# Kernel optimization log

Hardware: AMD Instinct MI355X
Metric: run time of the kernel (lower is better)

The kernel has to match this reference:

```python
import jax, jax.numpy as jnp
import numpy as np

H = 64  # hidden size
IN = 21  # input features

def setup_inputs() -> dict:
    key = jax.random.key(0)
    ks = jax.random.split(key, 12)
    s = 0.1
    B, T = 512, 3000
    return {
        "x":      jax.random.normal(ks[0], (B, T, IN), dtype=jnp.float32),
        # layer 0 (input 21 -> hidden 64); PyTorch gate order: i, f, g, o
        "Wih0":   jax.random.normal(ks[1], (4 * H, IN), dtype=jnp.float32) * s,
        "Whh0":   jax.random.normal(ks[2], (4 * H, H), dtype=jnp.float32) * s,
        "bih0":   jax.random.normal(ks[3], (4 * H,), dtype=jnp.float32) * s,
        "bhh0":   jax.random.normal(ks[4], (4 * H,), dtype=jnp.float32) * s,
        # layer 1 (hidden 64 -> hidden 64)
        "Wih1":   jax.random.normal(ks[5], (4 * H, H), dtype=jnp.float32) * s,
        "Whh1":   jax.random.normal(ks[6], (4 * H, H), dtype=jnp.float32) * s,
        "bih1":   jax.random.normal(ks[7], (4 * H,), dtype=jnp.float32) * s,
        "bhh1":   jax.random.normal(ks[8], (4 * H,), dtype=jnp.float32) * s,
        # final linear 64 -> 1
        "Wfc":    jax.random.normal(ks[9], (1, H), dtype=jnp.float32) * s,
        "bfc":    jax.random.normal(ks[10], (1,), dtype=jnp.float32) * s,
    }

def _lstm_layer(x_seq, Wih, Whh, bih, bhh):
    # x_seq: [B, T, F]. Precompute input projections for all timesteps (one big GEMM).
    xg = jnp.einsum('btf,gf->btg', x_seq, Wih) + (bih + bhh)  # [B, T, 4H]
    xg = jnp.transpose(xg, (1, 0, 2))  # [T, B, 4H] for scan over time
    B = x_seq.shape[0]
    h0 = jnp.zeros((B, H), dtype=x_seq.dtype)
    c0 = jnp.zeros((B, H), dtype=x_seq.dtype)

    def step(carry, xg_t):
        h, c = carry
        gates = xg_t + h @ Whh.T  # [B, 4H]
        i = jax.nn.sigmoid(gates[:, 0 * H:1 * H])
        f = jax.nn.sigmoid(gates[:, 1 * H:2 * H])
        g = jnp.tanh(gates[:, 2 * H:3 * H])
        o = jax.nn.sigmoid(gates[:, 3 * H:4 * H])
        c = f * c + i * g
        h = o * jnp.tanh(c)
        return (h, c), h

    (_, _), h_seq = jax.lax.scan(step, (h0, c0), xg)  # h_seq: [T, B, H]
    return jnp.transpose(h_seq, (1, 0, 2))  # [B, T, H]

def reference(x, Wih0, Whh0, bih0, bhh0, Wih1, Whh1, bih1, bhh1, Wfc, bfc):
    # 2-layer LSTM (eval mode: inter-layer dropout inactive), last timestep -> linear.
    h1 = _lstm_layer(x, Wih0, Whh0, bih0, bhh0)   # [B, T, H]
    h2 = _lstm_layer(h1, Wih1, Whh1, bih1, bhh1)  # [B, T, H]
    last = h2[:, -1, :]                            # [B, H]
    return last @ Wfc.T + bfc                      # [B, 1]
```

## Files before the change

### kernel.cpp

```cpp
#include <hip/hip_runtime.h>
#include <stdint.h>

namespace {

constexpr int NIN = 21;
constexpr int T   = 3000;
constexpr int NB  = 2;

typedef _Float16 f16x8 __attribute__((ext_vector_type(8)));
typedef float    f32x4 __attribute__((ext_vector_type(4)));

__device__ __forceinline__ float frcp(float x){ return __builtin_amdgcn_rcpf(x); }
__device__ __forceinline__ float sigm(float v){ return frcp(1.0f + __expf(-v)); }
__device__ __forceinline__ float tanh_fast(float v){
    return fmaf(-2.0f, frcp(__expf(2.0f*v) + 1.0f), 1.0f);
}

template<int CTRL>
__device__ __forceinline__ float dppf(float v){
    return __int_as_float(__builtin_amdgcn_update_dpp(
        0, __float_as_int(v), CTRL, 0xF, 0xF, true));
}
constexpr int SHR4  = 0x114;
constexpr int SHR8  = 0x118;
constexpr int SHR12 = 0x11C;
constexpr int ROR14 = 0x12E;

#define MFMA(A,B,C) __builtin_amdgcn_mfma_f32_16x16x32_f16((A),(B),(C),0,0,0)

__device__ __forceinline__ f16x8 ldfrag(const _Float16* p){
    return *reinterpret_cast<const f16x8*>(p);
}
__device__ __forceinline__ void cvt8h(const float* s, f16x8& hi){
    #pragma unroll
    for (int j=0;j<8;++j) hi[j] = (_Float16)s[j];
}

__launch_bounds__(512, 2)
__global__ void lstm_mf7(const float* __restrict__ x,
                         const float* __restrict__ Wih0, const float* __restrict__ Whh0,
                         const float* __restrict__ bih0, const float* __restrict__ bhh0,
                         const float* __restrict__ Wih1, const float* __restrict__ Whh1,
                         const float* __restrict__ bih1, const float* __restrict__ bhh1,
                         const float* __restrict__ Wfc,  const float* __restrict__ bfc,
                         float* __restrict__ out)
{
    const int tid  = threadIdx.x;
    const int lane = tid & 63;
    const int wid  = tid >> 6;
    const int c    = lane >> 4;
    const int mcol = lane & 15;
    const int b0   = blockIdx.x * NB;
    const bool isL0 = (wid < 4);
    const int  w    = wid & 3;

    __shared__ __align__(16) _Float16 h1p[2][2][NB][72];
    __shared__ __align__(16) _Float16 h2p[2][2][NB][72];
    __shared__ __align__(16) _Float16 xp [4][2][NB][40];

    f16x8 Whi[4][4];
    f32x4 bias4[4];
    {
        float tmp[8];
        #pragma unroll
        for (int tau = 0; tau < 4; ++tau) {
            const int n = 64*tau + 16*w + mcol;
            if (isL0) {
                #pragma unroll
                for (int j=0;j<8;++j){ int k=8*c+j; tmp[j] = (k<NIN)? Wih0[n*NIN+k] : 0.0f; }
                cvt8h(tmp, Whi[tau][0]);
                #pragma unroll
                for (int kc=0;kc<2;++kc){
                    #pragma unroll
                    for (int j=0;j<8;++j) tmp[j] = Whh0[n*64 + 32*kc + 8*c + j];
                    cvt8h(tmp, Whi[tau][1+kc]);
                }
                #pragma unroll
                for (int j=0;j<8;++j) Whi[tau][3][j] = (_Float16)0.f;
            } else {
                #pragma unroll
                for (int kc=0;kc<2;++kc){
                    #pragma unroll
                    for (int j=0;j<8;++j) tmp[j] = Wih1[n*64 + 32*kc + 8*c + j];
                    cvt8h(tmp, Whi[tau][kc]);
                }
                #pragma unroll
                for (int kc=0;kc<2;++kc){
                    #pragma unroll
                    for (int j=0;j<8;++j) tmp[j] = Whh1[n*64 + 32*kc + 8*c + j];
                    cvt8h(tmp, Whi[tau][2+kc]);
                }
            }
            const int nb = 64*tau + 16*w + 4*c;
            #pragma unroll
            for (int v=0; v<4; ++v)
                bias4[tau][v] = 0.5f * (isL0 ? (bih0[nb+v] + bhh0[nb+v])
                                             : (bih1[nb+v] + bhh1[nb+v]));
        }
    }

    {
        uint32_t* p1 = (uint32_t*)&h1p[0][0][0][0];
        uint32_t* p2 = (uint32_t*)&h2p[0][0][0][0];
        uint32_t* p3 = (uint32_t*)&xp[0][0][0][0];
        if (tid < 288){ p1[tid]=0u; p2[tid]=0u; }
        if (tid < 320){ p3[tid]=0u; }
    }
    __syncthreads();

    const bool stg = (wid < 2) && (lane < NIN);
    const float* xsrc = x + (size_t)(b0 + (wid & 1)) * T * NIN + lane;
    float xrA = 0.f, xrB = 0.f;
    if (stg){
        float x0 = xsrc[0], x1 = xsrc[NIN];
        _Float16 hh0 = (_Float16)x0;
        xp[0][0][wid][lane] = hh0;
        xp[0][1][wid][lane] = (_Float16)(x0 - (float)hh0);
        _Float16 hh1 = (_Float16)x1;
        xp[1][0][wid][lane] = hh1;
        xp[1][1][wid][lane] = (_Float16)(x1 - (float)hh1);
        xrA = xsrc[(size_t)2*NIN];
        xrB = xsrc[(size_t)3*NIN];
    }
    __syncthreads();

    f16x8 Bf[4];
    #pragma unroll
    for (int kc=0;kc<4;++kc)
        #pragma unroll
        for (int j=0;j<8;++j) Bf[kc][j] = (_Float16)0.f;
    if (isL0 && mcol < 4){
        Bf[0] = ldfrag(&xp[0][mcol>>1][mcol&1][8*c]);
    }

    float cst = 0.f;
    const int q   = mcol >> 2;
    const int m   = mcol & 1;
    const int pl  = (mcol >> 1) & 1;
    const int u   = 16*w + 4*c + q;
    const bool pw = ((mcol & 2) == 0);

    for (int tb = 0; tb < T; tb += 4) {
        #pragma unroll
        for (int ph = 0; ph < 4; ++ph) {
            const int t = tb + ph;
            float xnew = 0.f;
            if (stg && (t + 4 < T)) xnew = xsrc[(size_t)(t+4)*NIN];

            f32x4 a0 = bias4[0], a1 = bias4[1], a2 = bias4[2], a3 = bias4[3];
            if (isL0) {
                #pragma unroll
                for (int kc=0; kc<3; ++kc){
                    a0 = MFMA(Whi[0][kc], Bf[kc], a0);
                    a1 = MFMA(Whi[1][kc], Bf[kc], a1);
                    a2 = MFMA(Whi[2][kc], Bf[kc], a2);
                    a3 = MFMA(Whi[3][kc], Bf[kc], a3);
                }
            } else {
                #pragma unroll
                for (int kc=0; kc<4; ++kc){
                    a0 = MFMA(Whi[0][kc], Bf[kc], a0);
                    a1 = MFMA(Whi[1][kc], Bf[kc], a1);
                    a2 = MFMA(Whi[2][kc], Bf[kc], a2);
                    a3 = MFMA(Whi[3][kc], Bf[kc], a3);
                }
            }

            float g0, g1, g2, g3;
            {
                float u1, u2, u3;
                u1 = dppf<SHR4>(a0[1]); u2 = dppf<SHR8>(a0[2]); u3 = dppf<SHR12>(a0[3]);
                g0 = (q==0)? a0[0] : (q==1)? u1 : (q==2)? u2 : u3;
                u1 = dppf<SHR4>(a1[1]); u2 = dppf<SHR8>(a1[2]); u3 = dppf<SHR12>(a1[3]);
                g1 = (q==0)? a1[0] : (q==1)? u1 : (q==2)? u2 : u3;
                u1 = dppf<SHR4>(a2[1]); u2 = dppf<SHR8>(a2[2]); u3 = dppf<SHR12>(a2[3]);
                g2 = (q==0)? a2[0] : (q==1)? u1 : (q==2)? u2 : u3;
                u1 = dppf<SHR4>(a3[1]); u2 = dppf<SHR8>(a3[2]); u3 = dppf<SHR12>(a3[3]);
                g3 = (q==0)? a3[0] : (q==1)? u1 : (q==2)? u2 : u3;
                g0 += dppf<ROR14>(g0);
                g1 += dppf<ROR14>(g1);
                g2 += dppf<ROR14>(g2);
                g3 += dppf<ROR14>(g3);
            }

            const bool dow = pw && (isL0 || t > 0);
            _Float16 hh = (_Float16)0.f, hl = (_Float16)0.f;
            if (dow) {
                float i_ = sigm(g0), f_ = sigm(g1);
                float gg = tanh_fast(g2), o_ = sigm(g3);
                cst = fmaf(f_, cst, i_ * gg);
                float h = o_ * tanh_fast(cst);
                hh = (_Float16)h;
                hl = (_Float16)(h - (float)hh);
            }

            __syncthreads();

            if (dow) {
                if (isL0){
                    h1p[ph & 1][0][m][u] = hh;
                    h1p[ph & 1][1][m][u] = hl;
                } else {
                    h2p[(ph+1) & 1][0][m][u] = hh;
                    h2p[(ph+1) & 1][1][m][u] = hl;
                }
            }
            if (stg){
                if (t + 2 < T){
                    _Float16 xh = (_Float16)xrA;
                    xp[(ph+2) & 3][0][wid][lane] = xh;
                    xp[(ph+2) & 3][1][wid][lane] = (_Float16)(xrA - (float)xh);
                }
                xrA = xrB; xrB = xnew;
            }

            __syncthreads();

            if (mcol < 4){
                if (isL0){
                    Bf[0] = ldfrag(&xp[(ph+1) & 3][pl][m][8*c]);
                    Bf[1] = ldfrag(&h1p[ph & 1][pl][m][8*c]);
                    Bf[2] = ldfrag(&h1p[ph & 1][pl][m][32 + 8*c]);
                } else {
                    Bf[0] = ldfrag(&h1p[ph & 1][pl][m][8*c]);
                    Bf[1] = ldfrag(&h1p[ph & 1][pl][m][32 + 8*c]);
                    Bf[2] = ldfrag(&h2p[(ph+1) & 1][pl][m][8*c]);
                    Bf[3] = ldfrag(&h2p[(ph+1) & 1][pl][m][32 + 8*c]);
                }
            }
        }
    }

    if (!isL0) {
        f32x4 a0 = bias4[0], a1 = bias4[1], a2 = bias4[2], a3 = bias4[3];
        #pragma unroll
        for (int kc=0; kc<4; ++kc){
            a0 = MFMA(Whi[0][kc], Bf[kc], a0);
            a1 = MFMA(Whi[1][kc], Bf[kc], a1);
            a2 = MFMA(Whi[2][kc], Bf[kc], a2);
            a3 = MFMA(Whi[3][kc], Bf[kc], a3);
        }
        float g0, g1, g2, g3;
        {
            float u1, u2, u3;
            u1 = dppf<SHR4>(a0[1]); u2 = dppf<SHR8>(a0[2]); u3 = dppf<SHR12>(a0[3]);
            g0 = (q==0)? a0[0] : (q==1)? u1 : (q==2)? u2 : u3;
            u1 = dppf<SHR4>(a1[1]); u2 = dppf<SHR8>(a1[2]); u3 = dppf<SHR12>(a1[3]);
            g1 = (q==0)? a1[0] : (q==1)? u1 : (q==2)? u2 : u3;
            u1 = dppf<SHR4>(a2[1]); u2 = dppf<SHR8>(a2[2]); u3 = dppf<SHR12>(a2[3]);
            g2 = (q==0)? a2[0] : (q==1)? u1 : (q==2)? u2 : u3;
            u1 = dppf<SHR4>(a3[1]); u2 = dppf<SHR8>(a3[2]); u3 = dppf<SHR12>(a3[3]);
            g3 = (q==0)? a3[0] : (q==1)? u1 : (q==2)? u2 : u3;
            g0 += dppf<ROR14>(g0);
            g1 += dppf<ROR14>(g1);
            g2 += dppf<ROR14>(g2);
            g3 += dppf<ROR14>(g3);
        }
        if (pw) {
            float i_ = sigm(g0), f_ = sigm(g1);
            float gg = tanh_fast(g2), o_ = sigm(g3);
            cst = fmaf(f_, cst, i_ * gg);
            float h = o_ * tanh_fast(cst);
            _Float16 hh = (_Float16)h;
            h2p[(T-1) & 1][0][m][u] = hh;
            h2p[(T-1) & 1][1][m][u] = (_Float16)(h - (float)hh);
        }
    }
    __syncthreads();

    if (wid < NB) {
        float hv = (float)h2p[(T-1) & 1][0][wid][lane]
                 + (float)h2p[(T-1) & 1][1][wid][lane];
        float val = hv * Wfc[lane];
        #pragma unroll
        for (int off = 32; off > 0; off >>= 1)
            val += __shfl_down(val, off, 64);
        if (lane == 0) out[b0 + wid] = val + bfc[0];
    }
}

}

extern "C" void kernel_launch(void* const* d_in, const int* in_sizes, int n_in,
                              void* d_out, int out_size, void* d_ws, size_t ws_size,
                              hipStream_t stream)
{
    const float* x    = (const float*)d_in[0];
    const float* Wih0 = (const float*)d_in[1];
    const float* Whh0 = (const float*)d_in[2];
    const float* bih0 = (const float*)d_in[3];
    const float* bhh0 = (const float*)d_in[4];
    const float* Wih1 = (const float*)d_in[5];
    const float* Whh1 = (const float*)d_in[6];
    const float* bih1 = (const float*)d_in[7];
    const float* bhh1 = (const float*)d_in[8];
    const float* Wfc  = (const float*)d_in[9];
    const float* bfc  = (const float*)d_in[10];
    float* out = (float*)d_out;

    hipLaunchKernelGGL(lstm_mf7, dim3(512 / NB), dim3(512), 0, stream,
                       x, Wih0, Whh0, bih0, bhh0, Wih1, Whh1, bih1, bhh1,
                       Wfc, bfc, out);
}
```

Baseline: 1.859 ms.

## Issue layer-1 MFMAs after the barrier to overlap with layer-0 work

Layer-1 waves now run their gate MFMAs right after loading fragments at the end of each step, and do the activations at the start of the next step. This moves layer-1 matrix work off the path before the first barrier, so it overlaps with layer-0's MFMA and activation work. The layer-1 timeline gains one extra step of lag, so the epilogue adds an extra drain step and fixes the final buffer indices. The risk is higher register pressure from the carried accumulators and more complex index bookkeeping.

```diff
diff --git a/kernel.cpp b/kernel.cpp
--- a/kernel.cpp
+++ b/kernel.cpp
@@ -36,8 +36,27 @@
     for (int j=0;j<8;++j) hi[j] = (_Float16)s[j];
 }
 
+__device__ __forceinline__ void spread_fold(const f32x4& a0, const f32x4& a1,
+                                            const f32x4& a2, const f32x4& a3,
+                                            int q, float& g0, float& g1,
+                                            float& g2, float& g3){
+    float u1,u2,u3;
+    u1=dppf<SHR4>(a0[1]); u2=dppf<SHR8>(a0[2]); u3=dppf<SHR12>(a0[3]);
+    g0=(q==0)?a0[0]:(q==1)?u1:(q==2)?u2:u3;
+    u1=dppf<SHR4>(a1[1]); u2=dppf<SHR8>(a1[2]); u3=dppf<SHR12>(a1[3]);
+    g1=(q==0)?a1[0]:(q==1)?u1:(q==2)?u2:u3;
+    u1=dppf<SHR4>(a2[1]); u2=dppf<SHR8>(a2[2]); u3=dppf<SHR12>(a2[3]);
+    g2=(q==0)?a2[0]:(q==1)?u1:(q==2)?u2:u3;
+    u1=dppf<SHR4>(a3[1]); u2=dppf<SHR8>(a3[2]); u3=dppf<SHR12>(a3[3]);
+    g3=(q==0)?a3[0]:(q==1)?u1:(q==2)?u2:u3;
+    g0 += dppf<ROR14>(g0);
+    g1 += dppf<ROR14>(g1);
+    g2 += dppf<ROR14>(g2);
+    g3 += dppf<ROR14>(g3);
+}
+
 __launch_bounds__(512, 2)
-__global__ void lstm_mf7(const float* __restrict__ x,
+__global__ void lstm_mf8(const float* __restrict__ x,
                          const float* __restrict__ Wih0, const float* __restrict__ Whh0,
                          const float* __restrict__ bih0, const float* __restrict__ bhh0,
                          const float* __restrict__ Wih1, const float* __restrict__ Whh1,
@@ -140,130 +159,159 @@
     const int u   = 16*w + 4*c + q;
     const bool pw = ((mcol & 2) == 0);
 
+    f32x4 ac0 = {0,0,0,0}, ac1 = {0,0,0,0}, ac2 = {0,0,0,0}, ac3 = {0,0,0,0};
+
     for (int tb = 0; tb < T; tb += 4) {
         #pragma unroll
         for (int ph = 0; ph < 4; ++ph) {
             const int t = tb + ph;
             float xnew = 0.f;
-            if (stg && (t + 4 < T)) xnew = xsrc[(size_t)(t+4)*NIN];
-
-            f32x4 a0 = bias4[0], a1 = bias4[1], a2 = bias4[2], a3 = bias4[3];
+            _Float16 hh = (_Float16)0.f, hl = (_Float16)0.f;
+            bool dow = false;
+
             if (isL0) {
-                #pragma unroll
-                for (int kc=0; kc<3; ++kc){
+                if (stg && (t + 4 < T)) xnew = xsrc[(size_t)(t+4)*NIN];
+                f32x4 a0 = MFMA(Whi[0][0], Bf[0], bias4[0]);
+                f32x4 a1 = MFMA(Whi[1][0], Bf[0], bias4[1]);
+                f32x4 a2 = MFMA(Whi[2][0], Bf[0], bias4[2]);
+                f32x4 a3 = MFMA(Whi[3][0], Bf[0], bias4[3]);
+                #pragma unroll
+                for (int kc=1; kc<3; ++kc){
                     a0 = MFMA(Whi[0][kc], Bf[kc], a0);
                     a1 = MFMA(Whi[1][kc], Bf[kc], a1);
                     a2 = MFMA(Whi[2][kc], Bf[kc], a2);
                     a3 = MFMA(Whi[3][kc], Bf[kc], a3);
                 }
+                float g0,g1,g2,g3;
+                spread_fold(a0,a1,a2,a3,q,g0,g1,g2,g3);
+                if (pw) {
+                    float i_ = sigm(g0), f_ = sigm(g1);
+                    float gg = tanh_fast(g2), o_ = sigm(g3);
+                    cst = fmaf(f_, cst, i_ * gg);
+                    float h = o_ * tanh_fast(cst);
+                    hh = (_Float16)h;
+                    hl = (_Float16)(h - (float)hh);
+                    dow = true;
+                }
             } else {
-                #pragma unroll
-                for (int kc=0; kc<4; ++kc){
-                    a0 = MFMA(Whi[0][kc], Bf[kc], a0);
-                    a1 = MFMA(Whi[1][kc], Bf[kc], a1);
-                    a2 = MFMA(Whi[2][kc], Bf[kc], a2);
-                    a3 = MFMA(Whi[3][kc], Bf[kc], a3);
-                }
-            }
-
-            float g0, g1, g2, g3;
-            {
-                float u1, u2, u3;
-                u1 = dppf<SHR4>(a0[1]); u2 = dppf<SHR8>(a0[2]); u3 = dppf<SHR12>(a0[3]);
-                g0 = (q==0)? a0[0] : (q==1)? u1 : (q==2)? u2 : u3;
-                u1 = dppf<SHR4>(a1[1]); u2 = dppf<SHR8>(a1[2]); u3 = dppf<SHR12>(a1[3]);
-                g1 = (q==0)? a1[0] : (q==1)? u1 : (q==2)? u2 : u3;
-                u1 = dppf<SHR4>(a2[1]); u2 = dppf<SHR8>(a2[2]); u3 = dppf<SHR12>(a2[3]);
-                g2 = (q==0)? a2[0] : (q==1)? u1 : (q==2)? u2 : u3;
-                u1 = dppf<SHR4>(a3[1]); u2 = dppf<SHR8>(a3[2]); u3 = dppf<SHR12>(a3[3]);
-                g3 = (q==0)? a3[0] : (q==1)? u1 : (q==2)? u2 : u3;
-                g0 += dppf<ROR14>(g0);
-                g1 += dppf<ROR14>(g1);
-                g2 += dppf<ROR14>(g2);
-                g3 += dppf<ROR14>(g3);
-            }
-
-            const bool dow = pw && (isL0 || t > 0);
-            _Float16 hh = (_Float16)0.f, hl = (_Float16)0.f;
-            if (dow) {
+                if (t >= 2) {
+                    float g0,g1,g2,g3;
+                    spread_fold(ac0,ac1,ac2,ac3,q,g0,g1,g2,g3);
+                    if (pw) {
+                        float i_ = sigm(g0), f_ = sigm(g1);
+                        float gg = tanh_fast(g2), o_ = sigm(g3);
+                        cst = fmaf(f_, cst, i_ * gg);
+                        float h = o_ * tanh_fast(cst);
+                        hh = (_Float16)h;
+                        hl = (_Float16)(h - (float)hh);
+                        dow = true;
+                    }
+                }
+            }
+
+            __syncthreads();
+
+            if (isL0) {
+                if (dow) {
+                    h1p[ph & 1][0][m][u] = hh;
+                    h1p[ph & 1][1][m][u] = hl;
+                }
+                if (stg){
+                    if (t + 2 < T){
+                        _Float16 xh = (_Float16)xrA;
+                        xp[(ph+2) & 3][0][wid][lane] = xh;
+                        xp[(ph+2) & 3][1][wid][lane] = (_Float16)(xrA - (float)xh);
+                    }
+                    xrA = xrB; xrB = xnew;
+                }
+            } else if (dow) {
+                h2p[ph & 1][0][m][u] = hh;
+                h2p[ph & 1][1][m][u] = hl;
+            }
+
+            __syncthreads();
+
+            if (mcol < 4){
+                if (isL0){
+                    Bf[0] = ldfrag(&xp[(ph+1) & 3][pl][m][8*c]);
+                    Bf[1] = ldfrag(&h1p[ph & 1][pl][m][8*c]);
+                    Bf[2] = ldfrag(&h1p[ph & 1][pl][m][32 + 8*c]);
+                } else {
+                    Bf[0] = ldfrag(&h1p[(ph+1) & 1][pl][m][8*c]);
+                    Bf[1] = ldfrag(&h1p[(ph+1) & 1][pl][m][32 + 8*c]);
+                    Bf[2] = ldfrag(&h2p[ph & 1][pl][m][8*c]);
+                    Bf[3] = ldfrag(&h2p[ph & 1][pl][m][32 + 8*c]);
+                }
+            }
+            if (!isL0) {
+                ac0 = MFMA(Whi[0][0], Bf[0], bias4[0]);
+                ac1 = MFMA(Whi[1][0], Bf[0], bias4[1]);
+                ac2 = MFMA(Whi[2][0], Bf[0], bias4[2]);
+                ac3 = MFMA(Whi[3][0], Bf[0], bias4[3]);
+                #pragma unroll
+                for (int kc=1; kc<4; ++kc){
+                    ac0 = MFMA(Whi[0][kc], Bf[kc], ac0);
+                    ac1 = MFMA(Whi[1][kc], Bf[kc], ac1);
+                    ac2 = MFMA(Whi[2][kc], Bf[kc], ac2);
+                    ac3 = MFMA(Whi[3][kc], Bf[kc], ac3);
+                }
+            }
+        }
+    }
+
+    {
+        _Float16 hh = (_Float16)0.f, hl = (_Float16)0.f;
+        bool dow = false;
+        if (!isL0) {
+            float g0,g1,g2,g3;
+            spread_fold(ac0,ac1,ac2,ac3,q,g0,g1,g2,g3);
+            if (pw) {
                 float i_ = sigm(g0), f_ = sigm(g1);
                 float gg = tanh_fast(g2), o_ = sigm(g3);
                 cst = fmaf(f_, cst, i_ * gg);
                 float h = o_ * tanh_fast(cst);
                 hh = (_Float16)h;
                 hl = (_Float16)(h - (float)hh);
-            }
-
-            __syncthreads();
-
-            if (dow) {
-                if (isL0){
-                    h1p[ph & 1][0][m][u] = hh;
-                    h1p[ph & 1][1][m][u] = hl;
-                } else {
-                    h2p[(ph+1) & 1][0][m][u] = hh;
-                    h2p[(ph+1) & 1][1][m][u] = hl;
-                }
-            }
-            if (stg){
-                if (t + 2 < T){
-                    _Float16 xh = (_Float16)xrA;
-                    xp[(ph+2) & 3][0][wid][lane] = xh;
-                    xp[(ph+2) & 3][1][wid][lane] = (_Float16)(xrA - (float)xh);
-                }
-                xrA = xrB; xrB = xnew;
-            }
-
-            __syncthreads();
-
-            if (mcol < 4){
-                if (isL0){
-                    Bf[0] = ldfrag(&xp[(ph+1) & 3][pl][m][8*c]);
-                    Bf[1] = ldfrag(&h1p[ph & 1][pl][m][8*c]);
-                    Bf[2] = ldfrag(&h1p[ph & 1][pl][m][32 + 8*c]);
-                } else {
-                    Bf[0] = ldfrag(&h1p[ph & 1][pl][m][8*c]);
-                    Bf[1] = ldfrag(&h1p[ph & 1][pl][m][32 + 8*c]);
-                    Bf[2] = ldfrag(&h2p[(ph+1) & 1][pl][m][8*c]);
-                    Bf[3] = ldfrag(&h2p[(ph+1) & 1][pl][m][32 + 8*c]);
-                }
-            }
-        }
-    }
-
+                dow = true;
+            }
+        }
+        __syncthreads();
+        if (!isL0 && dow){
+            h2p[0][0][m][u] = hh;
+            h2p[0][1][m][u] = hl;
+        }
+        __syncthreads();
+        if (!isL0 && mcol < 4){
+            Bf[0] = ldfrag(&h1p[1][pl][m][8*c]);
+            Bf[1] = ldfrag(&h1p[1][pl][m][32 + 8*c]);
+            Bf[2] = ldfrag(&h2p[0][pl][m][8*c]);
+            Bf[3] = ldfrag(&h2p[0][pl][m][32 + 8*c]);
+        }
+        if (!isL0) {
+            ac0 = MFMA(Whi[0][0], Bf[0], bias4[0]);
+            ac1 = MFMA(Whi[1][0], Bf[0], bias4[1]);
+            ac2 = MFMA(Whi[2][0], Bf[0], bias4[2]);
+            ac3 = MFMA(Whi[3][0], Bf[0], bias4[3]);
+            #pragma unroll
+            for (int kc=1; kc<4; ++kc){
+                ac0 = MFMA(Whi[0][kc], Bf[kc], ac0);
+                ac1 = MFMA(Whi[1][kc], Bf[kc], ac1);
+                ac2 = MFMA(Whi[2][kc], Bf[kc], ac2);
+                ac3 = MFMA(Whi[3][kc], Bf[kc], ac3);
+            }
+        }
+    }
     if (!isL0) {
-        f32x4 a0 = bias4[0], a1 = bias4[1], a2 = bias4[2], a3 = bias4[3];
-        #pragma unroll
-        for (int kc=0; kc<4; ++kc){
-            a0 = MFMA(Whi[0][kc], Bf[kc], a0);
-            a1 = MFMA(Whi[1][kc], Bf[kc], a1);
-            a2 = MFMA(Whi[2][kc], Bf[kc], a2);
-            a3 = MFMA(Whi[3][kc], Bf[kc], a3);
-        }
-        float g0, g1, g2, g3;
-        {
-            float u1, u2, u3;
-            u1 = dppf<SHR4>(a0[1]); u2 = dppf<SHR8>(a0[2]); u3 = dppf<SHR12>(a0[3]);
-            g0 = (q==0)? a0[0] : (q==1)? u1 : (q==2)? u2 : u3;
-            u1 = dppf<SHR4>(a1[1]); u2 = dppf<SHR8>(a1[2]); u3 = dppf<SHR12>(a1[3]);
-            g1 = (q==0)? a1[0] : (q==1)? u1 : (q==2)? u2 : u3;
-            u1 = dppf<SHR4>(a2[1]); u2 = dppf<SHR8>(a2[2]); u3 = dppf<SHR12>(a2[3]);
-            g2 = (q==0)? a2[0] : (q==1)? u1 : (q==2)? u2 : u3;
-            u1 = dppf<SHR4>(a3[1]); u2 = dppf<SHR8>(a3[2]); u3 = dppf<SHR12>(a3[3]);
-            g3 = (q==0)? a3[0] : (q==1)? u1 : (q==2)? u2 : u3;
-            g0 += dppf<ROR14>(g0);
-            g1 += dppf<ROR14>(g1);
-            g2 += dppf<ROR14>(g2);
-            g3 += dppf<ROR14>(g3);
-        }
+        float g0,g1,g2,g3;
+        spread_fold(ac0,ac1,ac2,ac3,q,g0,g1,g2,g3);
         if (pw) {
             float i_ = sigm(g0), f_ = sigm(g1);
             float gg = tanh_fast(g2), o_ = sigm(g3);
             cst = fmaf(f_, cst, i_ * gg);
             float h = o_ * tanh_fast(cst);
             _Float16 hh = (_Float16)h;
-            h2p[(T-1) & 1][0][m][u] = hh;
-            h2p[(T-1) & 1][1][m][u] = (_Float16)(h - (float)hh);
+            h2p[1][0][m][u] = hh;
+            h2p[1][1][m][u] = (_Float16)(h - (float)hh);
         }
     }
     __syncthreads();
@@ -298,7 +346,7 @@
     const float* bfc  = (const float*)d_in[10];
     float* out = (float*)d_out;
 
-    hipLaunchKernelGGL(lstm_mf7, dim3(512 / NB), dim3(512), 0, stream,
+    hipLaunchKernelGGL(lstm_mf8, dim3(512 / NB), dim3(512), 0, stream,
                        x, Wih0, Whh0, bih0, bhh0, Wih1, Whh1, bih1, bhh1,
                        Wfc, bfc, out);
 }
```

New measurement: 1.980 ms. 1.07x slower.

## Drop one barrier per timestep using 4-deep LDS ring buffers

Applied to the files above, without the earlier changes.

The hidden-state buffers h1p and h2p grow from double- to quad-buffered, so each recurrent step needs only one block barrier instead of two. Writes for a step can no longer overwrite data that other waves are still reading. The remaining barrier is inline asm that waits only on LDS counters (lgkmcnt) and not on pending global loads, so the x prefetches, now held in a four-register queue, can stay in flight across it. This shortens the serial critical path of each step, at the cost of extra LDS and reliance on the ring depth for correctness.

```diff
diff --git a/kernel.cpp b/kernel.cpp
--- a/kernel.cpp
+++ b/kernel.cpp
@@ -28,6 +28,8 @@
 
 #define MFMA(A,B,C) __builtin_amdgcn_mfma_f32_16x16x32_f16((A),(B),(C),0,0,0)
 
+#define LDS_BARRIER() asm volatile("s_waitcnt lgkmcnt(0)\n\ts_barrier" ::: "memory")
+
 __device__ __forceinline__ f16x8 ldfrag(const _Float16* p){
     return *reinterpret_cast<const f16x8*>(p);
 }
@@ -36,8 +38,27 @@
     for (int j=0;j<8;++j) hi[j] = (_Float16)s[j];
 }
 
+__device__ __forceinline__ void spread_fold(const f32x4& a0, const f32x4& a1,
+                                            const f32x4& a2, const f32x4& a3,
+                                            int q, float& g0, float& g1,
+                                            float& g2, float& g3){
+    float u1,u2,u3;
+    u1=dppf<SHR4>(a0[1]); u2=dppf<SHR8>(a0[2]); u3=dppf<SHR12>(a0[3]);
+    g0=(q==0)?a0[0]:(q==1)?u1:(q==2)?u2:u3;
+    u1=dppf<SHR4>(a1[1]); u2=dppf<SHR8>(a1[2]); u3=dppf<SHR12>(a1[3]);
+    g1=(q==0)?a1[0]:(q==1)?u1:(q==2)?u2:u3;
+    u1=dppf<SHR4>(a2[1]); u2=dppf<SHR8>(a2[2]); u3=dppf<SHR12>(a2[3]);
+    g2=(q==0)?a2[0]:(q==1)?u1:(q==2)?u2:u3;
+    u1=dppf<SHR4>(a3[1]); u2=dppf<SHR8>(a3[2]); u3=dppf<SHR12>(a3[3]);
+    g3=(q==0)?a3[0]:(q==1)?u1:(q==2)?u2:u3;
+    g0 += dppf<ROR14>(g0);
+    g1 += dppf<ROR14>(g1);
+    g2 += dppf<ROR14>(g2);
+    g3 += dppf<ROR14>(g3);
+}
+
 __launch_bounds__(512, 2)
-__global__ void lstm_mf7(const float* __restrict__ x,
+__global__ void lstm_mf9(const float* __restrict__ x,
                          const float* __restrict__ Wih0, const float* __restrict__ Whh0,
                          const float* __restrict__ bih0, const float* __restrict__ bhh0,
                          const float* __restrict__ Wih1, const float* __restrict__ Whh1,
@@ -54,8 +75,8 @@
     const bool isL0 = (wid < 4);
     const int  w    = wid & 3;
 
-    __shared__ __align__(16) _Float16 h1p[2][2][NB][72];
-    __shared__ __align__(16) _Float16 h2p[2][2][NB][72];
+    __shared__ __align__(16) _Float16 h1p[4][2][NB][72];
+    __shared__ __align__(16) _Float16 h2p[4][2][NB][72];
     __shared__ __align__(16) _Float16 xp [4][2][NB][40];
 
     f16x8 Whi[4][4];
@@ -103,14 +124,14 @@
         uint32_t* p1 = (uint32_t*)&h1p[0][0][0][0];
         uint32_t* p2 = (uint32_t*)&h2p[0][0][0][0];
         uint32_t* p3 = (uint32_t*)&xp[0][0][0][0];
-        if (tid < 288){ p1[tid]=0u; p2[tid]=0u; }
-        if (tid < 320){ p3[tid]=0u; }
+        for (int i = tid; i < 576; i += 512){ p1[i]=0u; p2[i]=0u; }
+        if (tid < 320) p3[tid] = 0u;
     }
     __syncthreads();
 
     const bool stg = (wid < 2) && (lane < NIN);
     const float* xsrc = x + (size_t)(b0 + (wid & 1)) * T * NIN + lane;
-    float xrA = 0.f, xrB = 0.f;
+    float xq0 = 0.f, xq1 = 0.f, xq2 = 0.f, xq3 = 0.f;
     if (stg){
         float x0 = xsrc[0], x1 = xsrc[NIN];
         _Float16 hh0 = (_Float16)x0;
@@ -119,8 +140,8 @@
         _Float16 hh1 = (_Float16)x1;
         xp[1][0][wid][lane] = hh1;
         xp[1][1][wid][lane] = (_Float16)(x1 - (float)hh1);
-        xrA = xsrc[(size_t)2*NIN];
-        xrB = xsrc[(size_t)3*NIN];
+        xq2 = xsrc[(size_t)2*NIN];
+        xq3 = xsrc[(size_t)3*NIN];
     }
     __syncthreads();
 
@@ -144,47 +165,35 @@
         #pragma unroll
         for (int ph = 0; ph < 4; ++ph) {
             const int t = tb + ph;
-            float xnew = 0.f;
-            if (stg && (t + 4 < T)) xnew = xsrc[(size_t)(t+4)*NIN];
-
-            f32x4 a0 = bias4[0], a1 = bias4[1], a2 = bias4[2], a3 = bias4[3];
-            if (isL0) {
-                #pragma unroll
-                for (int kc=0; kc<3; ++kc){
-                    a0 = MFMA(Whi[0][kc], Bf[kc], a0);
-                    a1 = MFMA(Whi[1][kc], Bf[kc], a1);
-                    a2 = MFMA(Whi[2][kc], Bf[kc], a2);
-                    a3 = MFMA(Whi[3][kc], Bf[kc], a3);
-                }
-            } else {
-                #pragma unroll
-                for (int kc=0; kc<4; ++kc){
-                    a0 = MFMA(Whi[0][kc], Bf[kc], a0);
-                    a1 = MFMA(Whi[1][kc], Bf[kc], a1);
-                    a2 = MFMA(Whi[2][kc], Bf[kc], a2);
-                    a3 = MFMA(Whi[3][kc], Bf[kc], a3);
-                }
-            }
-
-            float g0, g1, g2, g3;
-            {
-                float u1, u2, u3;
-                u1 = dppf<SHR4>(a0[1]); u2 = dppf<SHR8>(a0[2]); u3 = dppf<SHR12>(a0[3]);
-                g0 = (q==0)? a0[0] : (q==1)? u1 : (q==2)? u2 : u3;
-                u1 = dppf<SHR4>(a1[1]); u2 = dppf<SHR8>(a1[2]); u3 = dppf<SHR12>(a1[3]);
-                g1 = (q==0)? a1[0] : (q==1)? u1 : (q==2)? u2 : u3;
-                u1 = dppf<SHR4>(a2[1]); u2 = dppf<SHR8>(a2[2]); u3 = dppf<SHR12>(a2[3]);
-                g2 = (q==0)? a2[0] : (q==1)? u1 : (q==2)? u2 : u3;
-                u1 = dppf<SHR4>(a3[1]); u2 = dppf<SHR8>(a3[2]); u3 = dppf<SHR12>(a3[3]);
-                g3 = (q==0)? a3[0] : (q==1)? u1 : (q==2)? u2 : u3;
-                g0 += dppf<ROR14>(g0);
-                g1 += dppf<ROR14>(g1);
-                g2 += dppf<ROR14>(g2);
-                g3 += dppf<ROR14>(g3);
-            }
-
+
+            if (stg && (t + 4 < T)) {
+                float v = xsrc[(size_t)(t+4)*NIN];
+                if (ph == 0) xq0 = v; else if (ph == 1) xq1 = v;
+                else if (ph == 2) xq2 = v; else xq3 = v;
+            }
+
+            f32x4 a0 = MFMA(Whi[0][0], Bf[0], bias4[0]);
+            f32x4 a1 = MFMA(Whi[1][0], Bf[0], bias4[1]);
+            f32x4 a2 = MFMA(Whi[2][0], Bf[0], bias4[2]);
+            f32x4 a3 = MFMA(Whi[3][0], Bf[0], bias4[3]);
+            #pragma unroll
+            for (int kc=1; kc<3; ++kc){
+                a0 = MFMA(Whi[0][kc], Bf[kc], a0);
+                a1 = MFMA(Whi[1][kc], Bf[kc], a1);
+                a2 = MFMA(Whi[2][kc], Bf[kc], a2);
+                a3 = MFMA(Whi[3][kc], Bf[kc], a3);
+            }
+            if (!isL0){
+                a0 = MFMA(Whi[0][3], Bf[3], a0);
+                a1 = MFMA(Whi[1][3], Bf[3], a1);
+                a2 = MFMA(Whi[2][3], Bf[3], a2);
+                a3 = MFMA(Whi[3][3], Bf[3], a3);
+            }
+            float g0,g1,g2,g3;
+            spread_fold(a0,a1,a2,a3,q,g0,g1,g2,g3);
+
+            _Float16 hh = (_Float16)0.f, hl = (_Float16)0.f;
             const bool dow = pw && (isL0 || t > 0);
-            _Float16 hh = (_Float16)0.f, hl = (_Float16)0.f;
             if (dow) {
                 float i_ = sigm(g0), f_ = sigm(g1);
                 float gg = tanh_fast(g2), o_ = sigm(g3);
@@ -194,83 +203,69 @@
                 hl = (_Float16)(h - (float)hh);
             }
 
-            __syncthreads();
-
             if (dow) {
                 if (isL0){
-                    h1p[ph & 1][0][m][u] = hh;
-                    h1p[ph & 1][1][m][u] = hl;
+                    h1p[ph & 3][0][m][u] = hh;
+                    h1p[ph & 3][1][m][u] = hl;
                 } else {
-                    h2p[(ph+1) & 1][0][m][u] = hh;
-                    h2p[(ph+1) & 1][1][m][u] = hl;
-                }
-            }
-            if (stg){
-                if (t + 2 < T){
-                    _Float16 xh = (_Float16)xrA;
-                    xp[(ph+2) & 3][0][wid][lane] = xh;
-                    xp[(ph+2) & 3][1][wid][lane] = (_Float16)(xrA - (float)xh);
-                }
-                xrA = xrB; xrB = xnew;
-            }
-
-            __syncthreads();
+                    h2p[(ph+3) & 3][0][m][u] = hh;
+                    h2p[(ph+3) & 3][1][m][u] = hl;
+                }
+            }
+            if (stg && (t + 2 < T)){
+                float xv = (ph == 0) ? xq2 : (ph == 1) ? xq3
+                         : (ph == 2) ? xq0 : xq1;
+                _Float16 xh = (_Float16)xv;
+                xp[(ph+2) & 3][0][wid][lane] = xh;
+                xp[(ph+2) & 3][1][wid][lane] = (_Float16)(xv - (float)xh);
+            }
+
+            LDS_BARRIER();
 
             if (mcol < 4){
                 if (isL0){
                     Bf[0] = ldfrag(&xp[(ph+1) & 3][pl][m][8*c]);
-                    Bf[1] = ldfrag(&h1p[ph & 1][pl][m][8*c]);
-                    Bf[2] = ldfrag(&h1p[ph & 1][pl][m][32 + 8*c]);
+                    Bf[1] = ldfrag(&h1p[ph & 3][pl][m][8*c]);
+                    Bf[2] = ldfrag(&h1p[ph & 3][pl][m][32 + 8*c]);
                 } else {
-                    Bf[0] = ldfrag(&h1p[ph & 1][pl][m][8*c]);
-                    Bf[1] = ldfrag(&h1p[ph & 1][pl][m][32 + 8*c]);
-                    Bf[2] = ldfrag(&h2p[(ph+1) & 1][pl][m][8*c]);
-                    Bf[3] = ldfrag(&h2p[(ph+1) & 1][pl][m][32 + 8*c]);
+                    Bf[0] = ldfrag(&h1p[ph & 3][pl][m][8*c]);
+                    Bf[1] = ldfrag(&h1p[ph & 3][pl][m][32 + 8*c]);
+                    Bf[2] = ldfrag(&h2p[(ph+3) & 3][pl][m][8*c]);
+                    Bf[3] = ldfrag(&h2p[(ph+3) & 3][pl][m][32 + 8*c]);
                 }
             }
         }
     }
 
     if (!isL0) {
-        f32x4 a0 = bias4[0], a1 = bias4[1], a2 = bias4[2], a3 = bias4[3];
-        #pragma unroll
-        for (int kc=0; kc<4; ++kc){
+        f32x4 a0 = MFMA(Whi[0][0], Bf[0], bias4[0]);
+        f32x4 a1 = MFMA(Whi[1][0], Bf[0], bias4[1]);
+        f32x4 a2 = MFMA(Whi[2][0], Bf[0], bias4[2]);
+        f32x4 a3 = MFMA(Whi[3][0], Bf[0], bias4[3]);
+        #pragma unroll
+        for (int kc=1; kc<4; ++kc){
             a0 = MFMA(Whi[0][kc], Bf[kc], a0);
             a1 = MFMA(Whi[1][kc], Bf[kc], a1);
             a2 = MFMA(Whi[2][kc], Bf[kc], a2);
             a3 = MFMA(Whi[3][kc], Bf[kc], a3);
         }
-        float g0, g1, g2, g3;
-        {
-            float u1, u2, u3;
-            u1 = dppf<SHR4>(a0[1]); u2 = dppf<SHR8>(a0[2]); u3 = dppf<SHR12>(a0[3]);
-            g0 = (q==0)? a0[0] : (q==1)? u1 : (q==2)? u2 : u3;
-            u1 = dppf<SHR4>(a1[1]); u2 = dppf<SHR8>(a1[2]); u3 = dppf<SHR12>(a1[3]);
-            g1 = (q==0)? a1[0] : (q==1)? u1 : (q==2)? u2 : u3;
-            u1 = dppf<SHR4>(a2[1]); u2 = dppf<SHR8>(a2[2]); u3 = dppf<SHR12>(a2[3]);
-            g2 = (q==0)? a2[0] : (q==1)? u1 : (q==2)? u2 : u3;
-            u1 = dppf<SHR4>(a3[1]); u2 = dppf<SHR8>(a3[2]); u3 = dppf<SHR12>(a3[3]);
-            g3 = (q==0)? a3[0] : (q==1)? u1 : (q==2)? u2 : u3;
-            g0 += dppf<ROR14>(g0);
-            g1 += dppf<ROR14>(g1);
-            g2 += dppf<ROR14>(g2);
-            g3 += dppf<ROR14>(g3);
-        }
+        float g0,g1,g2,g3;
+        spread_fold(a0,a1,a2,a3,q,g0,g1,g2,g3);
         if (pw) {
             float i_ = sigm(g0), f_ = sigm(g1);
             float gg = tanh_fast(g2), o_ = sigm(g3);
             cst = fmaf(f_, cst, i_ * gg);
             float h = o_ * tanh_fast(cst);
             _Float16 hh = (_Float16)h;
-            h2p[(T-1) & 1][0][m][u] = hh;
-            h2p[(T-1) & 1][1][m][u] = (_Float16)(h - (float)hh);
+            h2p[(T-1) & 3][0][m][u] = hh;
+            h2p[(T-1) & 3][1][m][u] = (_Float16)(h - (float)hh);
         }
     }
     __syncthreads();
 
     if (wid < NB) {
-        float hv = (float)h2p[(T-1) & 1][0][wid][lane]
-                 + (float)h2p[(T-1) & 1][1][wid][lane];
+        float hv = (float)h2p[(T-1) & 3][0][wid][lane]
+                 + (float)h2p[(T-1) & 3][1][wid][lane];
         float val = hv * Wfc[lane];
         #pragma unroll
         for (int off = 32; off > 0; off >>= 1)
@@ -298,7 +293,7 @@
     const float* bfc  = (const float*)d_in[10];
     float* out = (float*)d_out;
 
-    hipLaunchKernelGGL(lstm_mf7, dim3(512 / NB), dim3(512), 0, stream,
+    hipLaunchKernelGGL(lstm_mf9, dim3(512 / NB), dim3(512), 0, stream,
                        x, Wih0, Whh0, bih0, bhh0, Wih1, Whh1, bih1, bhh1,
                        Wfc, bfc, out);
 }
```

After: 1.668 ms (median of 2 runs). -10.3%, faster.
